# Kernel optimization log

Hardware: AMD Instinct MI355X
Metric: run time of the kernel (lower is better)

Reference implementation:

```python
import jax, jax.numpy as jnp
import numpy as np

V, E, H, NLAB, NL = 30000, 512, 256, 20, 2
B, T = 32, 512


def setup_inputs() -> dict:
    key = jax.random.key(0)
    ks = jax.random.split(key, 11)
    s = 0.05
    return {
        "input": jax.random.randint(ks[0], (B, T), 0, V, dtype=jnp.int32),
        "mask": jnp.ones((B, T), dtype=bool),
        "embed_table": jax.random.normal(ks[1], (V, E), jnp.float32) * s,
        "Wih": jax.random.normal(ks[2], (NL, 2, 4 * H, E), jnp.float32) * s,  # layer input dim E == 2H
        "Whh": jax.random.normal(ks[3], (NL, 2, 4 * H, H), jnp.float32) * s,
        "bias": jax.random.normal(ks[4], (NL, 2, 4 * H), jnp.float32) * s,  # b_ih + b_hh fused
        "lin_W": jax.random.normal(ks[5], (NLAB, 2 * H), jnp.float32) * s,
        "lin_b": jax.random.normal(ks[6], (NLAB,), jnp.float32) * s,
        "transitions": jax.random.normal(ks[7], (NLAB, NLAB), jnp.float32) * 0.1,
        "start_trans": jax.random.normal(ks[8], (NLAB,), jnp.float32) * 0.1,
        "end_trans": jax.random.normal(ks[9], (NLAB,), jnp.float32) * 0.1,
    }


def _lstm_dir(x, Wih, Whh, b, reverse):
    # x: [B,T,in] -> hs: [B,T,H]
    pre = jnp.swapaxes(x, 0, 1) @ Wih.T + b  # [T,B,4H] input projection precomputed
    h0 = jnp.zeros((x.shape[0], Whh.shape[1]), x.dtype)

    def step(carry, p):
        h, c = carry
        g = p + h @ Whh.T
        i, f, gg, o = jnp.split(g, 4, axis=-1)  # pytorch gate order i,f,g,o
        i = jax.nn.sigmoid(i); f = jax.nn.sigmoid(f)
        gg = jnp.tanh(gg); o = jax.nn.sigmoid(o)
        c = f * c + i * gg
        h = o * jnp.tanh(c)
        return (h, c), h

    _, hs = jax.lax.scan(step, (h0, h0), pre, reverse=reverse)
    return jnp.swapaxes(hs, 0, 1)


def _bilstm(x, Wih, Whh, bias):
    out = x
    for l in range(Wih.shape[0]):
        f = _lstm_dir(out, Wih[l, 0], Whh[l, 0], bias[l, 0], False)
        bwd = _lstm_dir(out, Wih[l, 1], Whh[l, 1], bias[l, 1], True)
        out = jnp.concatenate([f, bwd], axis=-1)
    return out


def _viterbi(em, mask, trans, start, end):
    # em: [B,T,L], mask: [B,T] (mask[:,0] assumed all True, as torchcrf requires)
    Bz, Tz, Lz = em.shape
    ar = jnp.arange(Lz, dtype=jnp.int32)
    score0 = start[None, :] + em[:, 0]

    def step(score, xs):
        em_t, m_t = xs  # [B,L], [B]
        ns = score[:, :, None] + trans[None] + em_t[:, None, :]  # [B,L_prev,L_cur]
        best = ns.max(axis=1)
        idx = ns.argmax(axis=1).astype(jnp.int32)
        score = jnp.where(m_t[:, None], best, score)
        idx = jnp.where(m_t[:, None], idx, ar[None, :])  # identity bp for padded steps
        return score, idx

    em_tb = jnp.swapaxes(em, 0, 1)
    m_tb = jnp.swapaxes(mask, 0, 1)
    score, hist = jax.lax.scan(step, score0, (em_tb[1:], m_tb[1:]))
    score = score + end[None, :]
    last = jnp.argmax(score, axis=-1).astype(jnp.int32)
    bidx = jnp.arange(Bz)

    def back(tag, bp):
        prev = bp[bidx, tag]
        return prev, prev

    _, prevs = jax.lax.scan(back, last, hist, reverse=True)  # prevs[t] = tag_t for t=0..T-2
    tags = jnp.concatenate([prevs, last[None]], axis=0)  # [T,B]
    return jnp.swapaxes(tags, 0, 1), score.max(axis=-1)


def reference(input, mask, embed_table, Wih, Whh, bias, lin_W, lin_b, transitions, start_trans, end_trans):
    x = embed_table[input]                      # [B,T,E]
    h = _bilstm(x, Wih, Whh, bias)              # [B,T,2H]
    em = h @ lin_W.T + lin_b                    # [B,T,L]
    tags, _ = _viterbi(em, mask, transitions, start_trans, end_trans)
    return tags
```

## Files before the change

kernel.cpp:

```cpp
#include <hip/hip_runtime.h>
#include <math.h>


#define T_SEQ   512
#define BATCH   32
#define HID     256
#define NLAB    20

#define AGENT __HIP_MEMORY_SCOPE_AGENT

__global__ __launch_bounds__(256) void prep_wih_k(const float* __restrict__ Wih,
                                                  const float* __restrict__ bias,
                                                  float* __restrict__ Wp,
                                                  float* __restrict__ bpp) {
  int idx = blockIdx.x * 256 + threadIdx.x;
  int k4 = idx & 127;
  int n  = (idx >> 7) & 1023;
  int ld = idx >> 17;
  int q = n & 3, j = n >> 2;
  int src = ld * 1024 + q * 256 + j;
  ((float4*)Wp)[idx] = ((const float4*)Wih)[(size_t)src * 128 + k4];
  if (k4 == 0) bpp[ld * 1024 + n] = bias[src];
}

__global__ __launch_bounds__(256) void prep_whh_reg_k(const float* __restrict__ Whh,
                                                      float4* __restrict__ Wreg) {
  int idx = blockIdx.x * 256 + threadIdx.x;
  int t  = idx & 511;
  int i  = (idx >> 9) & 31;
  int bx = (idx >> 14) & 3;
  int ld = idx >> 16;
  int kh = t & 1, lr = t >> 1;
  int n = bx * 256 + lr;
  int j = n >> 2, q = n & 3;
  int kb = kh * 128 + i * 4;
  Wreg[idx] = ((const float4*)Whh)[((size_t)(ld * 1024 + q * 256 + j) * 256 + kb) >> 2];
}

__global__ __launch_bounds__(256) void zero_hbuf_k(int4* __restrict__ p) {
  p[blockIdx.x * 256 + threadIdx.x] = int4{0, 0, 0, 0};
}

__global__ __launch_bounds__(256) void embed_k(const int* __restrict__ inp,
                                               const float* __restrict__ tab,
                                               float* __restrict__ x) {
  int idx = blockIdx.x * 256 + threadIdx.x;
  int row = idx >> 7, c = idx & 127;
  int tok = inp[row];
  ((float4*)x)[idx] = ((const float4*)tab)[(size_t)tok * 128 + c];
}

#define BM 64
#define BN 64
#define BKK 16
__global__ __launch_bounds__(256) void gemm_nt_k(const float* __restrict__ A,
                                                 const float* __restrict__ W,
                                                 const float* __restrict__ bias,
                                                 float* __restrict__ C,
                                                 int M, int N, int K) {
  __shared__ float As[BKK][BM];
  __shared__ float Ws[BKK][BN];
  int tid = threadIdx.x;
  int bm = blockIdx.x, bn = blockIdx.y;
  int r = tid >> 2, c4 = (tid & 3) * 4;
  int tm = (tid & 15) * 4, tn = (tid >> 4) * 4;
  const float* Ap = A + (size_t)(bm * BM + r) * K + c4;
  const float* Wq = W + (size_t)(bn * BN + r) * K + c4;
  float acc[4][4] = {};
  for (int k0 = 0; k0 < K; k0 += BKK) {
    float4 av = *(const float4*)(Ap + k0);
    float4 wv = *(const float4*)(Wq + k0);
    __syncthreads();
    As[c4 + 0][r] = av.x; As[c4 + 1][r] = av.y; As[c4 + 2][r] = av.z; As[c4 + 3][r] = av.w;
    Ws[c4 + 0][r] = wv.x; Ws[c4 + 1][r] = wv.y; Ws[c4 + 2][r] = wv.z; Ws[c4 + 3][r] = wv.w;
    __syncthreads();
#pragma unroll
    for (int kk = 0; kk < BKK; ++kk) {
      float4 a = *(const float4*)&As[kk][tm];
      float4 b = *(const float4*)&Ws[kk][tn];
      acc[0][0] += a.x * b.x; acc[0][1] += a.x * b.y; acc[0][2] += a.x * b.z; acc[0][3] += a.x * b.w;
      acc[1][0] += a.y * b.x; acc[1][1] += a.y * b.y; acc[1][2] += a.y * b.z; acc[1][3] += a.y * b.w;
      acc[2][0] += a.z * b.x; acc[2][1] += a.z * b.y; acc[2][2] += a.z * b.z; acc[2][3] += a.z * b.w;
      acc[3][0] += a.w * b.x; acc[3][1] += a.w * b.y; acc[3][2] += a.w * b.z; acc[3][3] += a.w * b.w;
    }
  }
  int m0 = bm * BM + tm, n0 = bn * BN + tn;
  float4 bv = *(const float4*)(bias + n0);
  float bb[4] = {bv.x, bv.y, bv.z, bv.w};
#pragma unroll
  for (int i = 0; i < 4; ++i)
#pragma unroll
    for (int jj = 0; jj < 4; ++jj)
      C[(size_t)(m0 + i) * N + n0 + jj] = acc[i][jj] + bb[jj];
}

__global__ __launch_bounds__(512, 2) void lstm_group_k(const float* __restrict__ pre,
                                                       const float4* __restrict__ WregL,
                                                       unsigned long long* __restrict__ hbuf,
                                                       float* __restrict__ Hout) {
  int raw = blockIdx.x;
  int xcd = raw & 7, slot = raw >> 3;
  int g  = xcd * 8 + (slot >> 2);
  int bx = slot & 3;
  int b = g >> 1, d = g & 1;
  int tid = threadIdx.x;
  int lr = tid >> 1, kh = tid & 1;

  __shared__ __align__(16) float hout_s[T_SEQ * 64];
  __shared__ __align__(16) float h_s[264];
  __shared__ __align__(16) float g_s[HID];

  float4 w[32];
  const float4* wp = WregL + ((size_t)(d * 4 + bx) * 32) * 512 + tid;
#pragma unroll
  for (int i = 0; i < 32; ++i) w[i] = wp[i * 512];

  unsigned long long* hb = hbuf + g * 512;
  const float* preB = pre + (size_t)b * T_SEQ * 2048 + d * 1024 + bx * 256 + lr;

  float c = 0.f;

  {
    int t = d ? (T_SEQ - 1) : 0;
    if ((tid & 1) == 0) g_s[lr] = preB[(size_t)t * 2048];
    __syncthreads();
    if (tid < 64) {
      float4 gg = *(const float4*)&g_s[4 * tid];
      float iv = 1.f / (1.f + expf(-gg.x));
      float fv = 1.f / (1.f + expf(-gg.y));
      float zv = tanhf(gg.z);
      float ov = 1.f / (1.f + expf(-gg.w));
      c = fv * c + iv * zv;
      float hn = ov * tanhf(c);
      hout_s[t * 64 + tid] = hn;
      unsigned long long pv = (1ULL << 32) | (unsigned long long)__float_as_uint(hn);
      __hip_atomic_store(&hb[256 + bx * 64 + tid], pv, __ATOMIC_RELAXED, AGENT);
    }
  }

  for (int s = 1; s < T_SEQ; ++s) {
    int t = d ? (T_SEQ - 1 - s) : s;
    float pre_v = preB[(size_t)t * 2048];

    if (tid < 256) {
      unsigned long long* hp = &hb[(s & 1) * 256 + tid];
      unsigned long long v;
      for (;;) {
        v = __hip_atomic_load(hp, __ATOMIC_RELAXED, AGENT);
        if (__all((unsigned)(v >> 32) == (unsigned)s)) break;
      }
      h_s[tid + ((tid >> 7) << 2)] = __uint_as_float((unsigned)v);
    }
    __syncthreads();

    const float* hbase = &h_s[kh * 132];
    float a0 = 0.f, a1 = 0.f, a2 = 0.f, a3 = 0.f;
#pragma unroll
    for (int i = 0; i < 32; ++i) {
      float4 h4 = *(const float4*)(hbase + 4 * i);
      a0 = fmaf(w[i].x, h4.x, a0);
      a1 = fmaf(w[i].y, h4.y, a1);
      a2 = fmaf(w[i].z, h4.z, a2);
      a3 = fmaf(w[i].w, h4.w, a3);
    }
    float acc = (a0 + a1) + (a2 + a3);
    acc += __shfl_xor(acc, 1);

    if ((tid & 1) == 0) g_s[lr] = acc + pre_v;
    __syncthreads();

    if (tid < 64) {
      float4 gg = *(const float4*)&g_s[4 * tid];
      float iv = 1.f / (1.f + expf(-gg.x));
      float fv = 1.f / (1.f + expf(-gg.y));
      float zv = tanhf(gg.z);
      float ov = 1.f / (1.f + expf(-gg.w));
      c = fv * c + iv * zv;
      float hn = ov * tanhf(c);
      hout_s[t * 64 + tid] = hn;
      if (s < T_SEQ - 1) {
        unsigned long long pv = ((unsigned long long)(unsigned)(s + 1) << 32) |
                                (unsigned long long)__float_as_uint(hn);
        __hip_atomic_store(&hb[((s + 1) & 1) * 256 + bx * 64 + tid], pv,
                           __ATOMIC_RELAXED, AGENT);
      }
    }
  }

  __syncthreads();
  const float4* src = (const float4*)hout_s;
  float4* dst = (float4*)Hout;
#pragma unroll
  for (int i = 0; i < 16; ++i) {
    int idx = i * 512 + tid;
    int t = idx >> 4, c4 = idx & 15;
    dst[((size_t)(b * T_SEQ + t) << 7) + d * 64 + bx * 16 + c4] = src[idx];
  }
}

__global__ __launch_bounds__(256) void linear20_k(const float* __restrict__ H,
                                                  const float* __restrict__ LW,
                                                  const float* __restrict__ lb,
                                                  float* __restrict__ em) {
  __shared__ float hs[8 * 516];
  __shared__ float lws[20 * 516];
  int tid = threadIdx.x;
  int m0 = blockIdx.x * 8;
  const float4* Hp = (const float4*)(H + (size_t)m0 * 512);
  for (int v = tid; v < 1024; v += 256) {
    int rr = v >> 7, cc = v & 127;
    *(float4*)&hs[rr * 516 + cc * 4] = Hp[v];
  }
  for (int v = tid; v < 2560; v += 256) {
    int ll = v >> 7, cc = v & 127;
    *(float4*)&lws[ll * 516 + cc * 4] = ((const float4*)LW)[v];
  }
  __syncthreads();
  if (tid < 160) {
    int rr = tid / 20, ll = tid % 20;
    float acc = 0.f;
    const float* hp = &hs[rr * 516];
    const float* wp = &lws[ll * 516];
#pragma unroll 8
    for (int k = 0; k < 512; ++k) acc += hp[k] * wp[k];
    em[(size_t)(m0 + rr) * 20 + ll] = acc + lb[ll];
  }
}

__global__ __launch_bounds__(640) void viterbi_k(const float* __restrict__ em,
                                                 const float* __restrict__ trans,
                                                 const float* __restrict__ startt,
                                                 const float* __restrict__ endt,
                                                 int* __restrict__ tags) {
  __shared__ float em_s[T_SEQ * NLAB];
  __shared__ float trans_s[NLAB * NLAB];
  __shared__ float score_s[NLAB];
  __shared__ unsigned char bp[(T_SEQ - 1) * NLAB];
  int b = blockIdx.x, tid = threadIdx.x;
  const float4* emb = (const float4*)(em + (size_t)b * T_SEQ * NLAB);
  for (int v = tid; v < T_SEQ * NLAB / 4; v += 640) ((float4*)em_s)[v] = emb[v];
  for (int v = tid; v < NLAB * NLAB; v += 640) trans_s[v] = trans[v];
  if (tid < NLAB) score_s[tid] = startt[tid] + em[(size_t)b * T_SEQ * NLAB + tid];
  __syncthreads();
  int j = tid >> 5;
  int i = tid & 31;
  float tr = (i < NLAB) ? trans_s[i * NLAB + j] : -1e30f;
  for (int t = 1; t < T_SEQ; ++t) {
    float v = (i < NLAB) ? (score_s[i] + tr) : -1e30f;
    int bi = i;
#pragma unroll
    for (int off = 16; off > 0; off >>= 1) {
      float ov = __shfl_down(v, off, 32);
      int oi = __shfl_down(bi, off, 32);
      if (ov > v || (ov == v && oi < bi)) { v = ov; bi = oi; }
    }
    __syncthreads();
    if (i == 0) {
      score_s[j] = v + em_s[t * NLAB + j];
      bp[(t - 1) * NLAB + j] = (unsigned char)bi;
    }
    __syncthreads();
  }
  if (tid == 0) {
    float best = score_s[0] + endt[0]; int cur = 0;
    for (int l = 1; l < NLAB; ++l) {
      float sv = score_s[l] + endt[l];
      if (sv > best) { best = sv; cur = l; }
    }
    int* tb = tags + b * T_SEQ;
    tb[T_SEQ - 1] = cur;
    for (int s2 = T_SEQ - 2; s2 >= 0; --s2) { cur = bp[s2 * NLAB + cur]; tb[s2] = cur; }
  }
}

extern "C" void kernel_launch(void* const* d_in, const int* in_sizes, int n_in,
                              void* d_out, int out_size, void* d_ws, size_t ws_size,
                              hipStream_t stream) {
  const int*   inp   = (const int*)d_in[0];
  const float* tab   = (const float*)d_in[2];
  const float* Wih   = (const float*)d_in[3];
  const float* Whh   = (const float*)d_in[4];
  const float* bias  = (const float*)d_in[5];
  const float* linW  = (const float*)d_in[6];
  const float* linb  = (const float*)d_in[7];
  const float* trans = (const float*)d_in[8];
  const float* stt   = (const float*)d_in[9];
  const float* endt  = (const float*)d_in[10];
  int* tags = (int*)d_out;

  float* ws   = (float*)d_ws;
  float* Wp   = ws;
  float* Wreg = Wp + 2097152;
  float* bpp  = Wreg + 1048576;
  float* x    = bpp + 4096;
  float* H0   = x + 8388608;
  float* pre  = H0 + 8388608;
  float* em   = pre + 33554432;
  unsigned long long* hbuf = (unsigned long long*)em;

  const float4* WregF4 = (const float4*)Wreg;

  hipLaunchKernelGGL(zero_hbuf_k, dim3(128), dim3(256), 0, stream, (int4*)hbuf);
  hipLaunchKernelGGL(prep_wih_k, dim3(2048), dim3(256), 0, stream, Wih, bias, Wp, bpp);
  hipLaunchKernelGGL(prep_whh_reg_k, dim3(1024), dim3(256), 0, stream, Whh, (float4*)Wreg);
  hipLaunchKernelGGL(embed_k, dim3(8192), dim3(256), 0, stream, inp, tab, x);

  const int M = BATCH * T_SEQ;
  hipLaunchKernelGGL(gemm_nt_k, dim3(M / BM, 2048 / BN), dim3(256), 0, stream,
                     x, Wp, bpp, pre, M, 2048, 512);
  hipLaunchKernelGGL(lstm_group_k, dim3(256), dim3(512), 0, stream,
                     pre, WregF4, hbuf, H0);
  hipLaunchKernelGGL(gemm_nt_k, dim3(M / BM, 2048 / BN), dim3(256), 0, stream,
                     H0, Wp + 2048 * 512, bpp + 2048, pre, M, 2048, 512);
  hipLaunchKernelGGL(lstm_group_k, dim3(256), dim3(512), 0, stream,
                     pre, WregF4 + 2 * 65536, hbuf + 32768, x);
  hipLaunchKernelGGL(linear20_k, dim3(M / 8), dim3(256), 0, stream, x, linW, linb, em);
  hipLaunchKernelGGL(viterbi_k, dim3(BATCH), dim3(640), 0, stream, em, trans, stt, endt, tags);
}
```

Before: 3.002 ms.

## Enlarge GEMM tiles with register prefetch; compute LSTM gates via shuffles

The input-projection GEMM moves from 64x64 to 128x128 tiles with 8x8 per-thread outputs, prefetching the next K slice into registers while computing, and storing results as float4. In the LSTM recurrence, gate values are gathered with wave shuffles inside each 8-lane group instead of going through shared memory, which drops one __syncthreads per timestep. h_s is double-buffered by step parity so the single remaining barrier per step is enough. All lanes now compute the nonlinearities redundantly, and the larger GEMM tile raises register pressure.

```diff
diff --git a/kernel.cpp b/kernel.cpp
--- a/kernel.cpp
+++ b/kernel.cpp
@@ -50,48 +50,74 @@
   ((float4*)x)[idx] = ((const float4*)tab)[(size_t)tok * 128 + c];
 }
 
-#define BM 64
-#define BN 64
-#define BKK 16
+#define GBM 128
+#define GBN 128
+#define GBK 16
 __global__ __launch_bounds__(256) void gemm_nt_k(const float* __restrict__ A,
                                                  const float* __restrict__ W,
                                                  const float* __restrict__ bias,
                                                  float* __restrict__ C,
                                                  int M, int N, int K) {
-  __shared__ float As[BKK][BM];
-  __shared__ float Ws[BKK][BN];
+  __shared__ float As[GBK][GBM];
+  __shared__ float Ws[GBK][GBN];
   int tid = threadIdx.x;
   int bm = blockIdx.x, bn = blockIdx.y;
-  int r = tid >> 2, c4 = (tid & 3) * 4;
-  int tm = (tid & 15) * 4, tn = (tid >> 4) * 4;
-  const float* Ap = A + (size_t)(bm * BM + r) * K + c4;
-  const float* Wq = W + (size_t)(bn * BN + r) * K + c4;
-  float acc[4][4] = {};
-  for (int k0 = 0; k0 < K; k0 += BKK) {
-    float4 av = *(const float4*)(Ap + k0);
-    float4 wv = *(const float4*)(Wq + k0);
-    __syncthreads();
-    As[c4 + 0][r] = av.x; As[c4 + 1][r] = av.y; As[c4 + 2][r] = av.z; As[c4 + 3][r] = av.w;
-    Ws[c4 + 0][r] = wv.x; Ws[c4 + 1][r] = wv.y; Ws[c4 + 2][r] = wv.z; Ws[c4 + 3][r] = wv.w;
-    __syncthreads();
-#pragma unroll
-    for (int kk = 0; kk < BKK; ++kk) {
-      float4 a = *(const float4*)&As[kk][tm];
-      float4 b = *(const float4*)&Ws[kk][tn];
-      acc[0][0] += a.x * b.x; acc[0][1] += a.x * b.y; acc[0][2] += a.x * b.z; acc[0][3] += a.x * b.w;
-      acc[1][0] += a.y * b.x; acc[1][1] += a.y * b.y; acc[1][2] += a.y * b.z; acc[1][3] += a.y * b.w;
-      acc[2][0] += a.z * b.x; acc[2][1] += a.z * b.y; acc[2][2] += a.z * b.z; acc[2][3] += a.z * b.w;
-      acc[3][0] += a.w * b.x; acc[3][1] += a.w * b.y; acc[3][2] += a.w * b.z; acc[3][3] += a.w * b.w;
-    }
-  }
-  int m0 = bm * BM + tm, n0 = bn * BN + tn;
-  float4 bv = *(const float4*)(bias + n0);
-  float bb[4] = {bv.x, bv.y, bv.z, bv.w};
-#pragma unroll
-  for (int i = 0; i < 4; ++i)
-#pragma unroll
-    for (int jj = 0; jj < 4; ++jj)
-      C[(size_t)(m0 + i) * N + n0 + jj] = acc[i][jj] + bb[jj];
+  int tm = (tid & 15) * 8, tn = (tid >> 4) * 8;
+  int r0 = tid >> 2, r1 = r0 + 64;
+  int c4 = (tid & 3) * 4;
+  const float* Ap = A + (size_t)(bm * GBM) * K + c4;
+  const float* Wq = W + (size_t)(bn * GBN) * K + c4;
+
+  float acc[8][8] = {};
+  float4 av0, av1, wv0, wv1;
+
+  av0 = *(const float4*)(Ap + (size_t)r0 * K);
+  av1 = *(const float4*)(Ap + (size_t)r1 * K);
+  wv0 = *(const float4*)(Wq + (size_t)r0 * K);
+  wv1 = *(const float4*)(Wq + (size_t)r1 * K);
+
+  for (int k0 = 0; k0 < K; k0 += GBK) {
+    __syncthreads();
+    As[c4 + 0][r0] = av0.x; As[c4 + 1][r0] = av0.y; As[c4 + 2][r0] = av0.z; As[c4 + 3][r0] = av0.w;
+    As[c4 + 0][r1] = av1.x; As[c4 + 1][r1] = av1.y; As[c4 + 2][r1] = av1.z; As[c4 + 3][r1] = av1.w;
+    Ws[c4 + 0][r0] = wv0.x; Ws[c4 + 1][r0] = wv0.y; Ws[c4 + 2][r0] = wv0.z; Ws[c4 + 3][r0] = wv0.w;
+    Ws[c4 + 0][r1] = wv1.x; Ws[c4 + 1][r1] = wv1.y; Ws[c4 + 2][r1] = wv1.z; Ws[c4 + 3][r1] = wv1.w;
+    __syncthreads();
+    if (k0 + GBK < K) {
+      int kn = k0 + GBK;
+      av0 = *(const float4*)(Ap + (size_t)r0 * K + kn);
+      av1 = *(const float4*)(Ap + (size_t)r1 * K + kn);
+      wv0 = *(const float4*)(Wq + (size_t)r0 * K + kn);
+      wv1 = *(const float4*)(Wq + (size_t)r1 * K + kn);
+    }
+#pragma unroll
+    for (int kk = 0; kk < GBK; ++kk) {
+      float a8[8], b8[8];
+      *(float4*)&a8[0] = *(const float4*)&As[kk][tm];
+      *(float4*)&a8[4] = *(const float4*)&As[kk][tm + 4];
+      *(float4*)&b8[0] = *(const float4*)&Ws[kk][tn];
+      *(float4*)&b8[4] = *(const float4*)&Ws[kk][tn + 4];
+#pragma unroll
+      for (int i = 0; i < 8; ++i)
+#pragma unroll
+        for (int j = 0; j < 8; ++j)
+          acc[i][j] = fmaf(a8[i], b8[j], acc[i][j]);
+    }
+  }
+
+  int m0 = bm * GBM + tm, n0 = bn * GBN + tn;
+  float4 bv0 = *(const float4*)(bias + n0);
+  float4 bv1 = *(const float4*)(bias + n0 + 4);
+#pragma unroll
+  for (int i = 0; i < 8; ++i) {
+    float4 o0, o1;
+    o0.x = acc[i][0] + bv0.x; o0.y = acc[i][1] + bv0.y;
+    o0.z = acc[i][2] + bv0.z; o0.w = acc[i][3] + bv0.w;
+    o1.x = acc[i][4] + bv1.x; o1.y = acc[i][5] + bv1.y;
+    o1.z = acc[i][6] + bv1.z; o1.w = acc[i][7] + bv1.w;
+    *(float4*)&C[(size_t)(m0 + i) * N + n0]     = o0;
+    *(float4*)&C[(size_t)(m0 + i) * N + n0 + 4] = o1;
+  }
 }
 
 __global__ __launch_bounds__(512, 2) void lstm_group_k(const float* __restrict__ pre,
@@ -105,10 +131,12 @@
   int b = g >> 1, d = g & 1;
   int tid = threadIdx.x;
   int lr = tid >> 1, kh = tid & 1;
+  int b8 = tid & ~7;
+  int myu = tid >> 3;
+  bool lead = (tid & 7) == 0;
 
   __shared__ __align__(16) float hout_s[T_SEQ * 64];
-  __shared__ __align__(16) float h_s[264];
-  __shared__ __align__(16) float g_s[HID];
+  __shared__ __align__(16) float h_s[2][264];
 
   float4 w[32];
   const float4* wp = WregL + ((size_t)(d * 4 + bx) * 32) * 512 + tid;
@@ -122,19 +150,21 @@
 
   {
     int t = d ? (T_SEQ - 1) : 0;
-    if ((tid & 1) == 0) g_s[lr] = preB[(size_t)t * 2048];
-    __syncthreads();
-    if (tid < 64) {
-      float4 gg = *(const float4*)&g_s[4 * tid];
-      float iv = 1.f / (1.f + expf(-gg.x));
-      float fv = 1.f / (1.f + expf(-gg.y));
-      float zv = tanhf(gg.z);
-      float ov = 1.f / (1.f + expf(-gg.w));
-      c = fv * c + iv * zv;
-      float hn = ov * tanhf(c);
-      hout_s[t * 64 + tid] = hn;
+    float acc = preB[(size_t)t * 2048];
+    float gi = __shfl(acc, b8 + 0, 64);
+    float gf = __shfl(acc, b8 + 2, 64);
+    float gg = __shfl(acc, b8 + 4, 64);
+    float go = __shfl(acc, b8 + 6, 64);
+    float iv = 1.f / (1.f + expf(-gi));
+    float fv = 1.f / (1.f + expf(-gf));
+    float zv = tanhf(gg);
+    float ov = 1.f / (1.f + expf(-go));
+    c = fv * c + iv * zv;
+    float hn = ov * tanhf(c);
+    if (lead) {
       unsigned long long pv = (1ULL << 32) | (unsigned long long)__float_as_uint(hn);
-      __hip_atomic_store(&hb[256 + bx * 64 + tid], pv, __ATOMIC_RELAXED, AGENT);
+      __hip_atomic_store(&hb[256 + bx * 64 + myu], pv, __ATOMIC_RELAXED, AGENT);
+      hout_s[t * 64 + myu] = hn;
     }
   }
 
@@ -149,11 +179,11 @@
         v = __hip_atomic_load(hp, __ATOMIC_RELAXED, AGENT);
         if (__all((unsigned)(v >> 32) == (unsigned)s)) break;
       }
-      h_s[tid + ((tid >> 7) << 2)] = __uint_as_float((unsigned)v);
-    }
-    __syncthreads();
-
-    const float* hbase = &h_s[kh * 132];
+      h_s[s & 1][tid + ((tid >> 7) << 2)] = __uint_as_float((unsigned)v);
+    }
+    __syncthreads();
+
+    const float* hbase = &h_s[s & 1][kh * 132];
     float a0 = 0.f, a1 = 0.f, a2 = 0.f, a3 = 0.f;
 #pragma unroll
     for (int i = 0; i < 32; ++i) {
@@ -165,25 +195,27 @@
     }
     float acc = (a0 + a1) + (a2 + a3);
     acc += __shfl_xor(acc, 1);
-
-    if ((tid & 1) == 0) g_s[lr] = acc + pre_v;
-    __syncthreads();
-
-    if (tid < 64) {
-      float4 gg = *(const float4*)&g_s[4 * tid];
-      float iv = 1.f / (1.f + expf(-gg.x));
-      float fv = 1.f / (1.f + expf(-gg.y));
-      float zv = tanhf(gg.z);
-      float ov = 1.f / (1.f + expf(-gg.w));
-      c = fv * c + iv * zv;
-      float hn = ov * tanhf(c);
-      hout_s[t * 64 + tid] = hn;
+    acc += pre_v;
+
+    float gi = __shfl(acc, b8 + 0, 64);
+    float gf = __shfl(acc, b8 + 2, 64);
+    float gg = __shfl(acc, b8 + 4, 64);
+    float go = __shfl(acc, b8 + 6, 64);
+    float iv = 1.f / (1.f + expf(-gi));
+    float fv = 1.f / (1.f + expf(-gf));
+    float zv = tanhf(gg);
+    float ov = 1.f / (1.f + expf(-go));
+    c = fv * c + iv * zv;
+    float hn = ov * tanhf(c);
+
+    if (lead) {
       if (s < T_SEQ - 1) {
         unsigned long long pv = ((unsigned long long)(unsigned)(s + 1) << 32) |
                                 (unsigned long long)__float_as_uint(hn);
-        __hip_atomic_store(&hb[((s + 1) & 1) * 256 + bx * 64 + tid], pv,
+        __hip_atomic_store(&hb[((s + 1) & 1) * 256 + bx * 64 + myu], pv,
                            __ATOMIC_RELAXED, AGENT);
       }
+      hout_s[t * 64 + myu] = hn;
     }
   }
 
@@ -306,11 +338,11 @@
   hipLaunchKernelGGL(embed_k, dim3(8192), dim3(256), 0, stream, inp, tab, x);
 
   const int M = BATCH * T_SEQ;
-  hipLaunchKernelGGL(gemm_nt_k, dim3(M / BM, 2048 / BN), dim3(256), 0, stream,
+  hipLaunchKernelGGL(gemm_nt_k, dim3(M / GBM, 2048 / GBN), dim3(256), 0, stream,
                      x, Wp, bpp, pre, M, 2048, 512);
   hipLaunchKernelGGL(lstm_group_k, dim3(256), dim3(512), 0, stream,
                      pre, WregF4, hbuf, H0);
-  hipLaunchKernelGGL(gemm_nt_k, dim3(M / BM, 2048 / BN), dim3(256), 0, stream,
+  hipLaunchKernelGGL(gemm_nt_k, dim3(M / GBM, 2048 / GBN), dim3(256), 0, stream,
                      H0, Wp + 2048 * 512, bpp + 2048, pre, M, 2048, 512);
   hipLaunchKernelGGL(lstm_group_k, dim3(256), dim3(512), 0, stream,
                      pre, WregF4 + 2 * 65536, hbuf + 32768, x);
```

Result: slower. 3.295 ms (+9.8%).
